# Optimization experiments

Measured on AMD Instinct MI355X. Metric: run time of the kernel, lower is better.

Reference implementation:

```python
import jax, jax.numpy as jnp
import numpy as np

N, D, V = 4096, 256, 32000
B, T = 32, 256
U_DECAY, X_DECAY = 0.97, 0.97
EPS = 1e-6


def layernorm_row(z):
    # matches torch: (z - mean) / (std + eps), std with Bessel correction (ddof=1)
    m = jnp.mean(z, axis=-1, keepdims=True)
    s = jnp.std(z, axis=-1, keepdims=True, ddof=1)
    return (z - m) / (s + EPS)


def setup_inputs() -> dict:
    key = jax.random.key(0)
    k1, k2, k3, k4, k5 = jax.random.split(key, 5)
    token_emb = jax.random.normal(k1, (V, D), jnp.float32) / np.float32(np.sqrt(D))
    E = jax.random.normal(k2, (D, N), jnp.float32) / np.float32(np.sqrt(N))
    Dx = jax.random.normal(k3, (N, D), jnp.float32) / np.float32(np.sqrt(D))
    Dy = jax.random.normal(k4, (N, D), jnp.float32) / np.float32(np.sqrt(D))
    idx = jax.random.randint(k5, (B, T), 0, V)
    return {"idx": idx, "token_emb": token_emb, "E": E, "Dx": Dx, "Dy": Dy}


def reference(idx, token_emb, E, Dx, Dy):
    b = idx.shape[0]

    def step(carry, tok):
        x, rho = carry                                   # x: (b,n), rho: (b,d,n)
        v_prev = token_emb[tok]                          # (b,d) embedding gather
        x_t = X_DECAY * x + jax.nn.relu(v_prev @ Dx.T)   # (b,n)
        x_t = x_t / (jnp.sum(jnp.abs(x_t), axis=-1, keepdims=True) + EPS)  # L1 normalize
        a_star = jnp.einsum('bdn,bn->bd', rho, x_t)      # fast-weight readout
        y_t = jax.nn.relu(layernorm_row(a_star) @ Dy.T) * jax.nn.relu(x_t)  # (b,n)
        v_star = layernorm_row(y_t @ E.T)                # (b,d)
        # Hebbian decayed outer-product memory update
        rho = U_DECAY * (rho + jnp.einsum('bd,bn->bdn', layernorm_row(v_prev), x_t))
        return (x_t, rho), v_star

    x0 = jnp.zeros((b, N), jnp.float32)
    rho0 = jnp.zeros((b, D, N), jnp.float32)
    (_, _), vs = jax.lax.scan(step, (x0, rho0), idx.T)   # vs: (T,b,d)
    return jnp.transpose(vs, (1, 0, 2))                  # (b,T,d)
```

## Files before the change

kernel.cpp:

```cpp
#include <hip/hip_runtime.h>
#include <hip/hip_bf16.h>

#define NN 4096
#define DD 256
#define BB 32
#define TT 256
#define EPS 1e-6f
#define DECAY 0.97f
#define LOG2_DECAY -0.043943348f

typedef __hip_bfloat16 bf16;
typedef short short8 __attribute__((ext_vector_type(8)));
typedef float floatx4 __attribute__((ext_vector_type(4)));

__device__ __forceinline__ float bfu2f(short u) {
    return __uint_as_float(((unsigned)(unsigned short)u) << 16);
}
__device__ __forceinline__ short f2bfu(float v) {
    bf16 t = __float2bfloat16(v);
    return *reinterpret_cast<short*>(&t);
}

__device__ __forceinline__ float blk_sum_256(float v, volatile float* s4) {
#pragma unroll
    for (int o = 32; o > 0; o >>= 1) v += __shfl_down(v, o, 64);
    int lane = threadIdx.x & 63, w = threadIdx.x >> 6;
    __syncthreads();
    if (lane == 0) s4[w] = v;
    __syncthreads();
    return s4[0] + s4[1] + s4[2] + s4[3];
}

__device__ __forceinline__ void gl16(const bf16* g, void* l) {
    __builtin_amdgcn_global_load_lds((const __attribute__((address_space(1))) void*)g,
                                     (__attribute__((address_space(3))) void*)l, 16, 0, 0);
}

__device__ __forceinline__ short8 frag64(const char* matbase, int row, int c) {
    return *(const short8*)(matbase + row * 128 + (((c) ^ (row & 7)) << 4));
}

__global__ void k_detect(const unsigned short* __restrict__ raw, int* __restrict__ flag) {
    __shared__ int cnt[4];
    int tid = threadIdx.x;
    int bad = 0;
    for (int i = tid; i < 8192; i += 256) {
        unsigned int u = raw[2 * i];
        float v = __uint_as_float(u << 16);
        if (!(fabsf(v) < 1e6f)) bad++;
    }
#pragma unroll
    for (int o = 32; o > 0; o >>= 1) bad += __shfl_down(bad, o, 64);
    int lane = tid & 63, w = tid >> 6;
    if (lane == 0) cnt[w] = bad;
    __syncthreads();
    if (tid == 0) flag[0] = (cnt[0] + cnt[1] + cnt[2] + cnt[3] < 32) ? 1 : 0;
}

__global__ __launch_bounds__(256) void k_convert3(const void* __restrict__ s0,
                                                  const void* __restrict__ s1,
                                                  const void* __restrict__ s2,
                                                  bf16* __restrict__ d0,
                                                  bf16* __restrict__ d1,
                                                  bf16* __restrict__ d2,
                                                  const int* __restrict__ flag) {
    const int per = NN * DD / 8;
    int i = blockIdx.x * 256 + threadIdx.x;
    int m = i / per, j = i % per;
    const void* s = (m == 0) ? s0 : (m == 1) ? s1 : s2;
    bf16* d = (m == 0) ? d0 : (m == 1) ? d1 : d2;
    if (flag[0]) {
        ((uint4*)d)[j] = ((const uint4*)s)[j];
    } else {
        const float4* f = (const float4*)s;
        float4 a = f[2 * j], b = f[2 * j + 1];
        short8 o;
        float va[8] = {a.x, a.y, a.z, a.w, b.x, b.y, b.z, b.w};
#pragma unroll
        for (int k = 0; k < 8; k++) o[k] = f2bfu(va[k]);
        ((short8*)d)[j] = o;
    }
}

__global__ __launch_bounds__(256) void k_gather_ln(const void* __restrict__ emb,
                                                   const int* __restrict__ idx,
                                                   bf16* __restrict__ Vpb,
                                                   bf16* __restrict__ Ub,
                                                   const int* __restrict__ flag) {
    __shared__ float s4[4];
    int r = blockIdx.x, d = threadIdx.x;
    int tok = idx[r];
    long o = (long)tok * DD + d;
    float e = flag[0] ? __bfloat162float(((const bf16*)emb)[o]) : ((const float*)emb)[o];
    Vpb[(long)r * DD + d] = __float2bfloat16(e);
    float m = blk_sum_256(e, s4) * (1.0f / DD);
    float zc = e - m;
    float var = blk_sum_256(zc * zc, s4) * (1.0f / (DD - 1));
    Ub[(long)r * DD + d] = __float2bfloat16(zc / (sqrtf(fmaxf(var, 0.f)) + EPS));
}

__global__ __launch_bounds__(256) void k_transpose(const bf16* __restrict__ Ub,
                                                   bf16* __restrict__ Ut) {
    __shared__ bf16 tile[32][33];
    int b = blockIdx.z;
    int t0 = blockIdx.x * 32, d0 = blockIdx.y * 32;
    const bf16* src = Ub + (long)b * TT * DD;
    bf16* dst = Ut + (long)b * DD * TT;
    int rr = threadIdx.x >> 3, c4 = (threadIdx.x & 7) * 4;
#pragma unroll
    for (int i = 0; i < 4; i++) tile[rr][c4 + i] = src[(long)(t0 + rr) * DD + d0 + c4 + i];
    __syncthreads();
#pragma unroll
    for (int i = 0; i < 4; i++) dst[(long)(d0 + rr) * TT + t0 + c4 + i] = tile[c4 + i][rr];
}

enum { EPI_RELU_BF16 = 0, EPI_RELU_MULX_BF16 = 2 };

template <int EPI>
__global__ __launch_bounds__(256) void k_g128(const bf16* __restrict__ A,
                                              const bf16* __restrict__ B,
                                              bf16* __restrict__ C,
                                              const bf16* __restrict__ Xaux,
                                              float* __restrict__ Wsum) {
    __shared__ __align__(16) char smem[32768];
    const int lda = DD, ldb = DD, ldc = NN;
    int bm = blockIdx.y * 128, bn = blockIdx.x * 128;
    int tid = threadIdx.x, w = tid >> 6, lane = tid & 63;
    int srow = lane >> 2, sch = lane & 3;

    floatx4 acc[4][4];
#pragma unroll
    for (int i = 0; i < 4; i++)
#pragma unroll
        for (int j = 0; j < 4; j++) acc[i][j] = (floatx4){0.f, 0.f, 0.f, 0.f};

#define STAGE32(buf, k0)                                                               \
    {                                                                                  \
        char* bb = smem + (buf)*16384;                                                 \
        _Pragma("unroll") for (int j = 0; j < 2; j++) {                                \
            int row = w * 32 + j * 16 + srow;                                          \
            gl16(A + (long)(bm + row) * lda + (k0) + sch * 8,                          \
                 bb + (w * 32 + j * 16) * 64 + lane * 16);                             \
            gl16(B + (long)(bn + row) * ldb + (k0) + sch * 8,                          \
                 bb + 8192 + (w * 32 + j * 16) * 64 + lane * 16);                      \
        }                                                                              \
    }

    int wm = (w >> 1) * 64, wn = (w & 1) * 64;
    int lm = lane & 15, kh = lane >> 4;

    STAGE32(0, 0);
#pragma unroll
    for (int it = 0; it < 8; it++) {
        __syncthreads();
        if (it < 7) STAGE32((it + 1) & 1, (it + 1) * 32);
        const char* Ab = smem + (it & 1) * 16384;
        const char* Bb = Ab + 8192;
        short8 af[4], bfr[4];
#pragma unroll
        for (int i = 0; i < 4; i++) af[i] = *(const short8*)(Ab + (wm + i * 16 + lm) * 64 + kh * 16);
#pragma unroll
        for (int j = 0; j < 4; j++) bfr[j] = *(const short8*)(Bb + (wn + j * 16 + lm) * 64 + kh * 16);
#pragma unroll
        for (int i = 0; i < 4; i++)
#pragma unroll
            for (int j = 0; j < 4; j++)
                acc[i][j] = __builtin_amdgcn_mfma_f32_16x16x32_bf16(af[i], bfr[j], acc[i][j], 0, 0, 0);
    }
#undef STAGE32

    bf16* R = (bf16*)smem;
#pragma unroll
    for (int p = 0; p < 2; p++) {
        __syncthreads();
        if ((w >> 1) == p) {
#pragma unroll
            for (int i = 0; i < 4; i++)
#pragma unroll
                for (int j = 0; j < 4; j++)
#pragma unroll
                    for (int r = 0; r < 4; r++) {
                        int rr = i * 16 + kh * 4 + r;
                        int cc = wn + j * 16 + lm;
                        R[rr * 136 + cc] = __float2bfloat16(fmaxf(acc[i][j][r], 0.f));
                    }
        }
        __syncthreads();
#pragma unroll
        for (int it2 = 0; it2 < 4; it2++) {
            int row_l = it2 * 16 + (tid >> 4);
            int c8 = (tid & 15) * 8;
            short8 vv = *(const short8*)(R + row_l * 136 + c8);
            int gm = bm + p * 64 + row_l;
            long off = (long)gm * ldc + bn + c8;
            if (EPI == EPI_RELU_BF16) {
                *(short8*)(C + off) = vv;
                float s = 0.f;
#pragma unroll
                for (int k = 0; k < 8; k++) s += bfu2f(vv[k]);
#pragma unroll
                for (int o = 8; o > 0; o >>= 1) s += __shfl_down(s, o, 16);
                if ((tid & 15) == 0) atomicAdd(&Wsum[gm], s);
            } else {
                short8 xx = *(const short8*)(Xaux + off);
                short8 oo;
#pragma unroll
                for (int k = 0; k < 8; k++) oo[k] = f2bfu(bfu2f(vv[k]) * fmaxf(bfu2f(xx[k]), 0.f));
                *(short8*)(C + off) = oo;
            }
        }
    }
}

template <int KITERS, int KSPLIT>
__global__ __launch_bounds__(256) void k_g64x128(const bf16* __restrict__ A, int lda, long sA,
                                                 const bf16* __restrict__ B, int ldb, long sB,
                                                 float* __restrict__ C, int ldc, long sC) {
    __shared__ __align__(16) char smem[49152];
    int z = blockIdx.z;
    int bz = z / KSPLIT, ks = z % KSPLIT;
    A += (long)bz * sA;
    B += (long)bz * sB;
    int kbase = ks * KITERS * 64;
    long cbase = (long)z * sC;
    int bm = blockIdx.y * 64, bn = blockIdx.x * 128;
    int tid = threadIdx.x, w = tid >> 6, lane = tid & 63;
    int lrow = lane >> 3, lph = lane & 7;
    int csw = lph ^ lrow;

    floatx4 acc[2][4];
#pragma unroll
    for (int i = 0; i < 2; i++)
#pragma unroll
        for (int j = 0; j < 4; j++) acc[i][j] = (floatx4){0.f, 0.f, 0.f, 0.f};

#define STAGE64128(buf, k0)                                                            \
    {                                                                                  \
        char* bb = smem + (buf)*24576;                                                 \
        _Pragma("unroll") for (int j = 0; j < 2; j++) {                                \
            int row = w * 16 + j * 8 + lrow;                                           \
            gl16(A + (long)(bm + row) * lda + (k0) + csw * 8,                          \
                 bb + (w * 16 + j * 8) * 128 + lane * 16);                             \
        }                                                                              \
        _Pragma("unroll") for (int j = 0; j < 4; j++) {                                \
            int row = w * 32 + j * 8 + lrow;                                           \
            gl16(B + (long)(bn + row) * ldb + (k0) + csw * 8,                          \
                 bb + 8192 + (w * 32 + j * 8) * 128 + lane * 16);                      \
        }                                                                              \
    }

    int wm = (w >> 1) * 32, wn = (w & 1) * 64;
    int lm = lane & 15, kh = lane >> 4;

    STAGE64128(0, kbase);
    for (int it = 0; it < KITERS; it++) {
        __syncthreads();
        if (it + 1 < KITERS) STAGE64128((it + 1) & 1, kbase + (it + 1) * 64);
        const char* Ab = smem + (it & 1) * 24576;
        const char* Bb = Ab + 8192;
#pragma unroll
        for (int ksu = 0; ksu < 2; ksu++) {
            int c = ksu * 4 + kh;
            short8 af[2], bfr[4];
#pragma unroll
            for (int i = 0; i < 2; i++) af[i] = frag64(Ab, wm + i * 16 + lm, c);
#pragma unroll
            for (int j = 0; j < 4; j++) bfr[j] = frag64(Bb, wn + j * 16 + lm, c);
#pragma unroll
            for (int i = 0; i < 2; i++)
#pragma unroll
                for (int j = 0; j < 4; j++)
                    acc[i][j] = __builtin_amdgcn_mfma_f32_16x16x32_bf16(af[i], bfr[j], acc[i][j], 0, 0, 0);
        }
    }
#undef STAGE64128

#pragma unroll
    for (int i = 0; i < 2; i++)
#pragma unroll
        for (int j = 0; j < 4; j++)
#pragma unroll
            for (int r = 0; r < 4; r++) {
                int gm = bm + wm + i * 16 + kh * 4 + r;
                int gn = bn + wn + j * 16 + lm;
                C[cbase + (long)gm * ldc + gn] = acc[i][j][r];
            }
}

__global__ __launch_bounds__(256) void k_scores(const bf16* __restrict__ X,
                                                float* __restrict__ Gp) {
    __shared__ __align__(16) char smem[32768];
    const int tri_i[10] = {0, 1, 1, 2, 2, 2, 3, 3, 3, 3};
    const int tri_j[10] = {0, 0, 1, 0, 1, 2, 0, 1, 2, 3};
    int z = blockIdx.z;
    int b = z >> 2, ks = z & 3;
    const bf16* A = X + (long)b * TT * NN;
    int kbase = ks * 1024;
    int bm = tri_i[blockIdx.x] * 64, bn = tri_j[blockIdx.x] * 64;
    int tid = threadIdx.x, w = tid >> 6, lane = tid & 63;
    int lrow = lane >> 3, lph = lane & 7;
    int csw = lph ^ lrow;

    floatx4 acc[2][2];
#pragma unroll
    for (int i = 0; i < 2; i++)
#pragma unroll
        for (int j = 0; j < 2; j++) acc[i][j] = (floatx4){0.f, 0.f, 0.f, 0.f};

#define STAGESC(buf, k0)                                                               \
    {                                                                                  \
        char* bb = smem + (buf)*16384;                                                 \
        _Pragma("unroll") for (int j = 0; j < 2; j++) {                                \
            int row = w * 16 + j * 8 + lrow;                                           \
            gl16(A + (long)(bm + row) * NN + (k0) + csw * 8,                           \
                 bb + (w * 16 + j * 8) * 128 + lane * 16);                             \
            gl16(A + (long)(bn + row) * NN + (k0) + csw * 8,                           \
                 bb + 8192 + (w * 16 + j * 8) * 128 + lane * 16);                      \
        }                                                                              \
    }

    int wm = (w >> 1) * 32, wn = (w & 1) * 32;
    int lm = lane & 15, kh = lane >> 4;

    STAGESC(0, kbase);
    for (int it = 0; it < 16; it++) {
        __syncthreads();
        if (it < 15) STAGESC((it + 1) & 1, kbase + (it + 1) * 64);
        const char* Ab = smem + (it & 1) * 16384;
        const char* Bb = Ab + 8192;
#pragma unroll
        for (int ksu = 0; ksu < 2; ksu++) {
            int c = ksu * 4 + kh;
            short8 af[2], bfr[2];
#pragma unroll
            for (int i = 0; i < 2; i++) af[i] = frag64(Ab, wm + i * 16 + lm, c);
#pragma unroll
            for (int j = 0; j < 2; j++) bfr[j] = frag64(Bb, wn + j * 16 + lm, c);
#pragma unroll
            for (int i = 0; i < 2; i++)
#pragma unroll
                for (int j = 0; j < 2; j++)
                    acc[i][j] = __builtin_amdgcn_mfma_f32_16x16x32_bf16(af[i], bfr[j], acc[i][j], 0, 0, 0);
        }
    }
#undef STAGESC

    float* Gb = Gp + ((long)b * 4 + ks) * 65536;
#pragma unroll
    for (int i = 0; i < 2; i++)
#pragma unroll
        for (int j = 0; j < 2; j++)
#pragma unroll
            for (int r = 0; r < 4; r++) {
                int gt = bm + wm + i * 16 + kh * 4 + r;
                int gs = bn + wn + j * 16 + lm;
                Gb[(long)gt * TT + gs] = acc[i][j][r];
            }
}

__global__ __launch_bounds__(256) void k_reduce_mask(const float* __restrict__ Gp,
                                                     bf16* __restrict__ G) {
    int r = blockIdx.x;
    int b = r >> 8, t = r & 255;
    int s = threadIdx.x;
    float o = 0.f;
    if (s < t) {
        long base = ((long)b * 4) * 65536 + (long)t * 256 + s;
        float v = Gp[base] + Gp[base + 65536] + Gp[base + 2 * 65536] + Gp[base + 3 * 65536];
        o = v * exp2f((float)(t - s) * LOG2_DECAY);
    }
    G[(long)r * 256 + s] = __float2bfloat16(o);
}

__global__ __launch_bounds__(256) void k_scalar_scan(const float* __restrict__ Wsum,
                                                     float* __restrict__ invS) {
    __shared__ float sw[BB * TT];
    for (int i = threadIdx.x; i < BB * TT; i += 256) sw[i] = Wsum[i];
    __syncthreads();
    int b = threadIdx.x;
    if (b < BB) {
        float sig = 0.f;
        for (int t = 0; t < TT; t++) {
            float S = DECAY * sig + sw[b * TT + t];
            float inv = 1.f / (S + EPS);
            invS[b * TT + t] = inv;
            sig = S * inv;
        }
    }
}

__global__ __launch_bounds__(256) void k_colscan(bf16* __restrict__ W,
                                                 const float* __restrict__ invS) {
    __shared__ float sv[TT];
    int b = blockIdx.y;
    sv[threadIdx.x] = invS[b * TT + threadIdx.x];
    __syncthreads();
    int n = blockIdx.x * 256 + threadIdx.x;
    bf16* p = W + (long)b * TT * NN + n;
    float x = 0.f;
    for (int t = 0; t < TT; t += 4) {
        short w0 = *(const short*)(p + (long)t * NN);
        short w1 = *(const short*)(p + (long)(t + 1) * NN);
        short w2 = *(const short*)(p + (long)(t + 2) * NN);
        short w3 = *(const short*)(p + (long)(t + 3) * NN);
        x = (DECAY * x + bfu2f(w0)) * sv[t];
        *(short*)(p + (long)t * NN) = f2bfu(x);
        x = (DECAY * x + bfu2f(w1)) * sv[t + 1];
        *(short*)(p + (long)(t + 1) * NN) = f2bfu(x);
        x = (DECAY * x + bfu2f(w2)) * sv[t + 2];
        *(short*)(p + (long)(t + 2) * NN) = f2bfu(x);
        x = (DECAY * x + bfu2f(w3)) * sv[t + 3];
        *(short*)(p + (long)(t + 3) * NN) = f2bfu(x);
    }
}

__global__ __launch_bounds__(256) void k_ln_rows(const float* __restrict__ Z,
                                                 bf16* __restrict__ O) {
    __shared__ float s4[4];
    long r = blockIdx.x;
    int d = threadIdx.x;
    float z = Z[r * DD + d];
    float m = blk_sum_256(z, s4) * (1.0f / DD);
    float zc = z - m;
    float var = blk_sum_256(zc * zc, s4) * (1.0f / (DD - 1));
    O[r * DD + d] = __float2bfloat16(zc / (sqrtf(fmaxf(var, 0.f)) + EPS));
}

__global__ __launch_bounds__(256) void k_final_ln(const float* __restrict__ Zp,
                                                  void* __restrict__ out,
                                                  const int* __restrict__ flag) {
    __shared__ float s4[4];
    long r = blockIdx.x;
    int d = threadIdx.x;
    const long SL = (long)8192 * 256;
    long o = r * DD + d;
    float z = Zp[o] + Zp[o + SL] + Zp[o + 2 * SL] + Zp[o + 3 * SL];
    float m = blk_sum_256(z, s4) * (1.0f / DD);
    float zc = z - m;
    float var = blk_sum_256(zc * zc, s4) * (1.0f / (DD - 1));
    float v = zc / (sqrtf(fmaxf(var, 0.f)) + EPS);
    if (flag[0]) ((bf16*)out)[o] = __float2bfloat16(v);
    else ((float*)out)[o] = v;
}

extern "C" void kernel_launch(void* const* d_in, const int* in_sizes, int n_in,
                              void* d_out, int out_size, void* d_ws, size_t ws_size,
                              hipStream_t stream) {
    const int* idx = (const int*)d_in[0];
    const void* emb = d_in[1];
    const void* E = d_in[2];
    const void* Dx = d_in[3];
    const void* Dy = d_in[4];

    char* base = (char*)d_ws;
    size_t off = 0;
    int* flag = (int*)base; off += 1024;
    bf16* Dxb = (bf16*)(base + off); off += (size_t)NN * DD * 2;
    bf16* Dyb = (bf16*)(base + off); off += (size_t)NN * DD * 2;
    bf16* Eb  = (bf16*)(base + off); off += (size_t)DD * NN * 2;
    bf16* Vpb = (bf16*)(base + off); off += (size_t)BB * TT * DD * 2;
    bf16* Ub  = (bf16*)(base + off); off += (size_t)BB * TT * DD * 2;
    bf16* Ut  = (bf16*)(base + off); off += (size_t)BB * TT * DD * 2;
    float* Wsum = (float*)(base + off); off += (size_t)BB * TT * 4;
    float* invS = (float*)(base + off); off += (size_t)BB * TT * 4;
    bf16* ALNb = (bf16*)(base + off); off += (size_t)BB * TT * DD * 2;
    bf16* G = (bf16*)(base + off); off += (size_t)BB * TT * TT * 2;
    float* Gp = (float*)(base + off); off += (size_t)4 * BB * TT * TT * 4;
    float* Zp = Gp;
    float* Astar = (float*)(base + off); off += (size_t)BB * TT * DD * 4;
    bf16* Xb = (bf16*)(base + off); off += (size_t)BB * TT * NN * 2;

    const int M = BB * TT;

    k_detect<<<1, 256, 0, stream>>>((const unsigned short*)emb, flag);
    k_convert3<<<3 * NN * DD / 8 / 256, 256, 0, stream>>>(Dx, Dy, E, Dxb, Dyb, Eb, flag);
    k_gather_ln<<<M, 256, 0, stream>>>(emb, idx, Vpb, Ub, flag);
    k_transpose<<<dim3(8, 8, BB), 256, 0, stream>>>(Ub, Ut);

    hipMemsetAsync(Wsum, 0, (size_t)M * 4, stream);

    k_g128<EPI_RELU_BF16><<<dim3(NN / 128, M / 128, 1), 256, 0, stream>>>(
        Vpb, Dxb, Xb, nullptr, Wsum);

    k_scalar_scan<<<1, 256, 0, stream>>>(Wsum, invS);
    k_colscan<<<dim3(NN / 256, BB, 1), 256, 0, stream>>>(Xb, invS);

    k_scores<<<dim3(10, 1, BB * 4), 256, 0, stream>>>(Xb, Gp);
    k_reduce_mask<<<M, 256, 0, stream>>>(Gp, G);

    k_g64x128<4, 1><<<dim3(DD / 128, TT / 64, BB), 256, 0, stream>>>(
        G, TT, (long)TT * TT, Ut, TT, (long)DD * TT, Astar, DD, (long)TT * DD);
    k_ln_rows<<<M, 256, 0, stream>>>(Astar, ALNb);

    k_g128<EPI_RELU_MULX_BF16><<<dim3(NN / 128, M / 128, 1), 256, 0, stream>>>(
        ALNb, Dyb, Xb, Xb, nullptr);

    k_g64x128<16, 4><<<dim3(DD / 128, M / 64, 4), 256, 0, stream>>>(
        Xb, NN, 0, Eb, NN, 0, Zp, DD, (long)M * DD);

    k_final_ln<<<M, 256, 0, stream>>>(Zp, d_out, flag);
}
```

Before: 344.5 us.

## Fuse score reduction and decay mask into attention GEMM; swizzle k_g128 LDS layout

Replaces the separate reduce-mask kernel and bf16 G buffer with a fused kernel that sums the four split-K score partials, applies the causal decay mask, converts to bf16 in registers, and feeds an MFMA GEMM against Ut. This removes one launch and a full write plus re-read of the G matrix. Separately, the k_g128 GEMM's LDS staging and fragment reads now use an XOR-swizzled layout to reduce bank conflicts. In exchange, the fused kernel reads the fp32 partials once per d-column block (two blocks), recomputes exp2 per element, and uses a single-buffered loop with no overlap of loads and compute.

```diff
diff --git a/kernel.cpp b/kernel.cpp
--- a/kernel.cpp
+++ b/kernel.cpp
@@ -126,7 +126,9 @@
     const int lda = DD, ldb = DD, ldc = NN;
     int bm = blockIdx.y * 128, bn = blockIdx.x * 128;
     int tid = threadIdx.x, w = tid >> 6, lane = tid & 63;
-    int srow = lane >> 2, sch = lane & 3;
+    int lsw = (lane & 7) ^ (lane >> 3);
+    int csel = lsw & 3;
+    int rsub = 2 * (lane >> 3) + (lsw >> 2);
 
     floatx4 acc[4][4];
 #pragma unroll
@@ -138,16 +140,18 @@
     {                                                                                  \
         char* bb = smem + (buf)*16384;                                                 \
         _Pragma("unroll") for (int j = 0; j < 2; j++) {                                \
-            int row = w * 32 + j * 16 + srow;                                          \
-            gl16(A + (long)(bm + row) * lda + (k0) + sch * 8,                          \
-                 bb + (w * 32 + j * 16) * 64 + lane * 16);                             \
-            gl16(B + (long)(bn + row) * ldb + (k0) + sch * 8,                          \
-                 bb + 8192 + (w * 32 + j * 16) * 64 + lane * 16);                      \
+            int base_r = w * 32 + j * 16;                                              \
+            gl16(A + (long)(bm + base_r + rsub) * lda + (k0) + csel * 8,               \
+                 bb + base_r * 64 + lane * 16);                                        \
+            gl16(B + (long)(bn + base_r + rsub) * ldb + (k0) + csel * 8,               \
+                 bb + 8192 + base_r * 64 + lane * 16);                                 \
         }                                                                              \
     }
 
     int wm = (w >> 1) * 64, wn = (w & 1) * 64;
     int lm = lane & 15, kh = lane >> 4;
+    int lmh = lm >> 1, lml = lm & 1;
+    int pq = ((lml << 2) + kh) ^ lmh;
 
     STAGE32(0, 0);
 #pragma unroll
@@ -158,9 +162,11 @@
         const char* Bb = Ab + 8192;
         short8 af[4], bfr[4];
 #pragma unroll
-        for (int i = 0; i < 4; i++) af[i] = *(const short8*)(Ab + (wm + i * 16 + lm) * 64 + kh * 16);
-#pragma unroll
-        for (int j = 0; j < 4; j++) bfr[j] = *(const short8*)(Bb + (wn + j * 16 + lm) * 64 + kh * 16);
+        for (int i = 0; i < 4; i++)
+            af[i] = *(const short8*)(Ab + (wm + i * 16) * 64 + lmh * 128 + pq * 16);
+#pragma unroll
+        for (int j = 0; j < 4; j++)
+            bfr[j] = *(const short8*)(Bb + (wn + j * 16) * 64 + lmh * 128 + pq * 16);
 #pragma unroll
         for (int i = 0; i < 4; i++)
 #pragma unroll
@@ -358,18 +364,97 @@
             }
 }
 
-__global__ __launch_bounds__(256) void k_reduce_mask(const float* __restrict__ Gp,
-                                                     bf16* __restrict__ G) {
-    int r = blockIdx.x;
-    int b = r >> 8, t = r & 255;
-    int s = threadIdx.x;
-    float o = 0.f;
-    if (s < t) {
-        long base = ((long)b * 4) * 65536 + (long)t * 256 + s;
-        float v = Gp[base] + Gp[base + 65536] + Gp[base + 2 * 65536] + Gp[base + 3 * 65536];
-        o = v * exp2f((float)(t - s) * LOG2_DECAY);
-    }
-    G[(long)r * 256 + s] = __float2bfloat16(o);
+__global__ __launch_bounds__(256) void k_attn(const float* __restrict__ Gp,
+                                              const bf16* __restrict__ Ut,
+                                              float* __restrict__ Astar) {
+    __shared__ __align__(16) char smem[24576];
+    int b = blockIdx.z;
+    int bm = blockIdx.y * 64;
+    int bn = blockIdx.x * 128;
+    int tid = threadIdx.x, w = tid >> 6, lane = tid & 63;
+    int lrow = lane >> 3, lph = lane & 7;
+    int csw = lph ^ lrow;
+
+    int arow = tid >> 2;
+    int aseg = (tid & 3) * 16;
+    int tglob = bm + arow;
+    const float* gp0 = Gp + (long)b * 4 * 65536 + (long)tglob * 256;
+    const bf16* Utb = Ut + (long)b * DD * TT;
+
+    floatx4 acc[2][4];
+#pragma unroll
+    for (int i = 0; i < 2; i++)
+#pragma unroll
+        for (int j = 0; j < 4; j++) acc[i][j] = (floatx4){0.f, 0.f, 0.f, 0.f};
+
+    int wm = (w >> 1) * 32, wn = (w & 1) * 64;
+    int lm = lane & 15, kh = lane >> 4;
+    char* Ab = smem;
+    char* Bb = smem + 8192;
+
+    for (int it = 0; it < 4; it++) {
+        int s0 = it * 64;
+        float vs[16];
+#pragma unroll
+        for (int e = 0; e < 16; e += 4) {
+            float4 p0 = *(const float4*)(gp0 + 0 * 65536 + s0 + aseg + e);
+            float4 p1 = *(const float4*)(gp0 + 1 * 65536 + s0 + aseg + e);
+            float4 p2 = *(const float4*)(gp0 + 2 * 65536 + s0 + aseg + e);
+            float4 p3 = *(const float4*)(gp0 + 3 * 65536 + s0 + aseg + e);
+            vs[e + 0] = p0.x + p1.x + p2.x + p3.x;
+            vs[e + 1] = p0.y + p1.y + p2.y + p3.y;
+            vs[e + 2] = p0.z + p1.z + p2.z + p3.z;
+            vs[e + 3] = p0.w + p1.w + p2.w + p3.w;
+        }
+        short8 sa, sb;
+#pragma unroll
+        for (int e = 0; e < 8; e++) {
+            int s = s0 + aseg + e;
+            sa[e] = f2bfu((s < tglob) ? vs[e] * exp2f((float)(tglob - s) * LOG2_DECAY) : 0.f);
+        }
+#pragma unroll
+        for (int e = 0; e < 8; e++) {
+            int s = s0 + aseg + 8 + e;
+            sb[e] = f2bfu((s < tglob) ? vs[8 + e] * exp2f((float)(tglob - s) * LOG2_DECAY) : 0.f);
+        }
+        __syncthreads();
+        {
+            int c0 = (tid & 3) * 2;
+            *(short8*)(Ab + arow * 128 + ((c0 ^ (arow & 7)) << 4)) = sa;
+            *(short8*)(Ab + arow * 128 + (((c0 + 1) ^ (arow & 7)) << 4)) = sb;
+        }
+#pragma unroll
+        for (int j = 0; j < 4; j++) {
+            int row = w * 32 + j * 8 + lrow;
+            gl16(Utb + (long)(bn + row) * TT + s0 + csw * 8, Bb + row * 128 + lane * 16);
+        }
+        __syncthreads();
+#pragma unroll
+        for (int ksu = 0; ksu < 2; ksu++) {
+            int c = ksu * 4 + kh;
+            short8 af[2], bfr[4];
+#pragma unroll
+            for (int i = 0; i < 2; i++) af[i] = frag64(Ab, wm + i * 16 + lm, c);
+#pragma unroll
+            for (int j = 0; j < 4; j++) bfr[j] = frag64(Bb, wn + j * 16 + lm, c);
+#pragma unroll
+            for (int i = 0; i < 2; i++)
+#pragma unroll
+                for (int j = 0; j < 4; j++)
+                    acc[i][j] = __builtin_amdgcn_mfma_f32_16x16x32_bf16(af[i], bfr[j], acc[i][j], 0, 0, 0);
+        }
+    }
+
+#pragma unroll
+    for (int i = 0; i < 2; i++)
+#pragma unroll
+        for (int j = 0; j < 4; j++)
+#pragma unroll
+            for (int r = 0; r < 4; r++) {
+                int gt = bm + wm + i * 16 + kh * 4 + r;
+                int gd = bn + wn + j * 16 + lm;
+                Astar[((long)b * TT + gt) * DD + gd] = acc[i][j][r];
+            }
 }
 
 __global__ __launch_bounds__(256) void k_scalar_scan(const float* __restrict__ Wsum,
@@ -464,7 +549,6 @@
     float* Wsum = (float*)(base + off); off += (size_t)BB * TT * 4;
     float* invS = (float*)(base + off); off += (size_t)BB * TT * 4;
     bf16* ALNb = (bf16*)(base + off); off += (size_t)BB * TT * DD * 2;
-    bf16* G = (bf16*)(base + off); off += (size_t)BB * TT * TT * 2;
     float* Gp = (float*)(base + off); off += (size_t)4 * BB * TT * TT * 4;
     float* Zp = Gp;
     float* Astar = (float*)(base + off); off += (size_t)BB * TT * DD * 4;
@@ -486,10 +570,8 @@
     k_colscan<<<dim3(NN / 256, BB, 1), 256, 0, stream>>>(Xb, invS);
 
     k_scores<<<dim3(10, 1, BB * 4), 256, 0, stream>>>(Xb, Gp);
-    k_reduce_mask<<<M, 256, 0, stream>>>(Gp, G);
-
-    k_g64x128<4, 1><<<dim3(DD / 128, TT / 64, BB), 256, 0, stream>>>(
-        G, TT, (long)TT * TT, Ut, TT, (long)DD * TT, Astar, DD, (long)TT * DD);
+
+    k_attn<<<dim3(DD / 128, TT / 64, BB), 256, 0, stream>>>(Gp, Ut, Astar);
     k_ln_rows<<<M, 256, 0, stream>>>(Astar, ALNb);
 
     k_g128<EPI_RELU_MULX_BF16><<<dim3(NN / 128, M / 128, 1), 256, 0, stream>>>(
```

Result: no change. 348.8 us (+1.3%).
